# Kernel optimization log

Measured on AMD Instinct MI355X. Metric: run time of the kernel, lower is better.

## Reference

```python
import jax, jax.numpy as jnp
import numpy as np

B, S, D, H = 2, 2048, 1024, 16
DK = D // H
NEG = -1.0e9

def setup_inputs() -> dict:
    key = jax.random.key(0)
    ks = jax.random.split(key, 12)
    sc = 1.0 / np.sqrt(D)
    q = jax.random.normal(ks[0], (B, S, D), jnp.float32)
    k = jax.random.normal(ks[1], (B, S, D), jnp.float32)
    v = jax.random.normal(ks[2], (B, S, D), jnp.float32)
    # causal mask: True = masked (matches masked_fill(mask == True, -1e9))
    mask = jnp.broadcast_to(jnp.triu(jnp.ones((S, S), bool), k=1)[None, None], (B, 1, S, S))
    Wq = jax.random.normal(ks[3], (D, D), jnp.float32) * sc
    bq = jnp.zeros((D,), jnp.float32)
    Wk = jax.random.normal(ks[4], (D, D), jnp.float32) * sc
    bk = jnp.zeros((D,), jnp.float32)
    Wv = jax.random.normal(ks[5], (D, D), jnp.float32) * sc
    bv = jnp.zeros((D,), jnp.float32)
    Wo = jax.random.normal(ks[6], (D, D), jnp.float32) * sc
    bo = jnp.zeros((D,), jnp.float32)
    return {"q": q, "k": k, "v": v, "mask": mask,
            "Wq": Wq, "bq": bq, "Wk": Wk, "bk": bk,
            "Wv": Wv, "bv": bv, "Wo": Wo, "bo": bo}

def reference(q, k, v, mask, Wq, bq, Wk, bk, Wv, bv, Wo, bo):
    def split_heads(x):  # [B,S,D] -> [B,H,S,DK]
        return x.reshape(B, S, H, DK).transpose(0, 2, 1, 3)
    qh = split_heads(q @ Wq + bq)
    kh = split_heads(k @ Wk + bk)
    vh = split_heads(v @ Wv + bv)
    scores = jnp.einsum('bhqd,bhkd->bhqk', qh, kh) / np.sqrt(DK)
    scores = jnp.where(mask, NEG, scores)
    p = jax.nn.softmax(scores, axis=-1)
    out = jnp.einsum('bhqk,bhkd->bhqd', p, vh)  # [B,H,S,DK]
    out = out.transpose(0, 2, 1, 3).reshape(B, S, D)
    return out @ Wo + bo
```

## Files before the change

kernel.cpp:

```cpp
#include <hip/hip_runtime.h>

#define BB 2
#define SS 2048
#define DD 1024
#define HH 16
#define DKK 64

typedef __attribute__((ext_vector_type(8))) short short8;
typedef __attribute__((ext_vector_type(4))) float floatx4;

__device__ inline float bf2f(ushort u) {
    union { unsigned int i; float f; } x; x.i = ((unsigned int)u) << 16; return x.f;
}
__device__ inline ushort f2bf(float f) {
    union { float f; unsigned int i; } x; x.f = f;
    unsigned int r = x.i + 0x7fff + ((x.i >> 16) & 1);
    return (ushort)(r >> 16);
}
__device__ inline void async_cp16(const ushort* g, ushort* l) {
    __builtin_amdgcn_global_load_lds(
        (const __attribute__((address_space(1))) unsigned int*)g,
        (__attribute__((address_space(3))) unsigned int*)l, 16, 0, 0);
}
__device__ inline unsigned int cvt_pk_bf16(float lo, float hi) {
    unsigned int r;
    asm("v_cvt_pk_bf16_f32 %0, %1, %2" : "=v"(r) : "v"(lo), "v"(hi));
    return r;
}
__device__ inline void swap32(unsigned int& a, unsigned int& b) {
    asm("v_permlane32_swap_b32 %0, %1" : "+v"(a), "+v"(b));
}
__device__ inline void swap16(unsigned int& a, unsigned int& b) {
    asm("v_permlane16_swap_b32 %0, %1" : "+v"(a), "+v"(b));
}

__global__ __launch_bounds__(256) void cvt_w4(const float* __restrict__ w0,
                                              const float* __restrict__ w1,
                                              const float* __restrict__ w2,
                                              const float* __restrict__ w3,
                                              ushort* __restrict__ o0,
                                              ushort* __restrict__ o1,
                                              ushort* __restrict__ o2,
                                              ushort* __restrict__ o3) {
    __shared__ ushort t[32][33];
    int z = blockIdx.z;
    const float* in = (z == 0) ? w0 : (z == 1) ? w1 : (z == 2) ? w2 : w3;
    ushort* out = (z == 0) ? o0 : (z == 1) ? o1 : (z == 2) ? o2 : o3;
    int bx = blockIdx.x, by = blockIdx.y, tx = threadIdx.x;
    for (int i = threadIdx.y; i < 32; i += 8)
        t[i][tx] = f2bf(in[(size_t)(by * 32 + i) * DD + bx * 32 + tx]);
    __syncthreads();
    for (int i = threadIdx.y; i < 32; i += 8)
        out[(size_t)(bx * 32 + i) * DD + by * 32 + tx] = t[tx][i];
}

__global__ __launch_bounds__(256) void cvt_qkv(const float* __restrict__ q,
                                               const float* __restrict__ k,
                                               const float* __restrict__ v,
                                               ushort* __restrict__ oq,
                                               ushort* __restrict__ ok,
                                               ushort* __restrict__ ov) {
    int z = blockIdx.z;
    const float* in = (z == 0) ? q : (z == 1) ? k : v;
    ushort* out = (z == 0) ? oq : (z == 1) ? ok : ov;
    int i = blockIdx.x * 256 + threadIdx.x;
    float4 f0 = ((const float4*)in)[i * 2];
    float4 f1 = ((const float4*)in)[i * 2 + 1];
    short8 p;
    p[0] = (short)f2bf(f0.x); p[1] = (short)f2bf(f0.y);
    p[2] = (short)f2bf(f0.z); p[3] = (short)f2bf(f0.w);
    p[4] = (short)f2bf(f1.x); p[5] = (short)f2bf(f1.y);
    p[6] = (short)f2bf(f1.z); p[7] = (short)f2bf(f1.w);
    ((short8*)out)[i] = p;
}

__global__ __launch_bounds__(256) void gemm_qkv(const ushort* __restrict__ Xq,
                                                const ushort* __restrict__ Xk,
                                                const ushort* __restrict__ Xv,
                                                const ushort* __restrict__ WtQ,
                                                const ushort* __restrict__ WtK,
                                                const ushort* __restrict__ WtV,
                                                const float* __restrict__ bq,
                                                const float* __restrict__ bk,
                                                const float* __restrict__ bv,
                                                ushort* __restrict__ qh,
                                                ushort* __restrict__ kh,
                                                ushort* __restrict__ vt) {
    constexpr int K = 1024;
    constexpr int LDT = 136;
    __shared__ ushort smem[128 * LDT];
    ushort* Asm = smem;
    ushort* Bsm = smem + 4096;

    int lin = blockIdx.x + ((blockIdx.y + (blockIdx.z << 5)) << 3);
    int wid = (lin & 7) * 96 + (lin >> 3);
    int z = wid >> 8;
    int rem = wid & 255;
    int by = rem >> 3, bx = rem & 7;

    const ushort* A  = (z == 0) ? Xq : (z == 1) ? Xk : Xv;
    const ushort* Bt = (z == 0) ? WtQ : (z == 1) ? WtK : WtV;
    const float* bias = (z == 0) ? bq : (z == 1) ? bk : bv;
    ushort* outp = (z == 0) ? qh : (z == 1) ? kh : vt;

    int tid = threadIdx.x;
    int wave = tid >> 6, lane = tid & 63, quad = lane >> 4, l15 = lane & 15;
    int wm = wave >> 1, wn = wave & 1;
    int rowBase = by * 128, colBase = bx * 128;

    floatx4 acc[4][4] = {};
    for (int k0 = 0; k0 < K; k0 += 32) {
#pragma unroll
        for (int j = 0; j < 2; ++j) {
            int cbase = (j * 4 + wave) * 64;
            int c = cbase + lane;
            int row = c >> 2, sub = (c & 3) * 8;
            async_cp16(&A[(size_t)(rowBase + row) * K + k0 + sub], &Asm[cbase * 8]);
            async_cp16(&Bt[(size_t)(colBase + row) * K + k0 + sub], &Bsm[cbase * 8]);
        }
        __syncthreads();
        short8 af[4], bf[4];
#pragma unroll
        for (int mi = 0; mi < 4; ++mi)
            af[mi] = *(const short8*)&Asm[(wm * 64 + mi * 16 + l15) * 32 + quad * 8];
#pragma unroll
        for (int ni = 0; ni < 4; ++ni)
            bf[ni] = *(const short8*)&Bsm[(wn * 64 + ni * 16 + l15) * 32 + quad * 8];
#pragma unroll
        for (int mi = 0; mi < 4; ++mi)
#pragma unroll
            for (int ni = 0; ni < 4; ++ni)
                acc[mi][ni] = __builtin_amdgcn_mfma_f32_16x16x32_bf16(
                    af[mi], bf[ni], acc[mi][ni], 0, 0, 0);
        __syncthreads();
    }
    if (z == 2) {
        for (int mi = 0; mi < 4; ++mi)
            for (int ni = 0; ni < 4; ++ni) {
                int c = wn * 64 + ni * 16 + l15;
                float bv = bias[colBase + c];
                for (int i = 0; i < 4; ++i) {
                    int r = wm * 64 + mi * 16 + quad * 4 + i;
                    smem[c * LDT + r] = f2bf(acc[mi][ni][i] + bv);
                }
            }
        __syncthreads();
        int b = rowBase >> 11;
        int sBase = rowBase & 2047;
#pragma unroll
        for (int u = 0; u < 8; ++u) {
            int chunk = u * 256 + tid;
            int c = chunk >> 4;
            int r = (chunk & 15) * 8;
            int col = colBase + c, h = col >> 6, dk = col & 63;
            int4 val = *(const int4*)&smem[c * LDT + r];
            *(int4*)&outp[((size_t)((b * HH + h) * DKK + dk)) * SS + sBase + r] = val;
        }
    } else {
        for (int mi = 0; mi < 4; ++mi)
            for (int ni = 0; ni < 4; ++ni) {
                int c = wn * 64 + ni * 16 + l15;
                float bv = bias[colBase + c];
                for (int i = 0; i < 4; ++i) {
                    int r = wm * 64 + mi * 16 + quad * 4 + i;
                    smem[r * LDT + c] = f2bf(acc[mi][ni][i] + bv);
                }
            }
        __syncthreads();
        int bb = rowBase >> 11;
        int sBase = rowBase & 2047;
#pragma unroll
        for (int u = 0; u < 8; ++u) {
            int chunk = u * 256 + tid;
            int r = chunk >> 4;
            int cc = (chunk & 15) * 8;
            int col = colBase + cc, hh = col >> 6, dk = col & 63;
            int4 val = *(const int4*)&smem[r * LDT + cc];
            *(int4*)&outp[((size_t)((bb * HH + hh) * SS + sBase + r)) * DKK + dk] = val;
        }
    }
}

__global__ __launch_bounds__(256) void gemm_fin(const ushort* __restrict__ A,
                                                const ushort* __restrict__ Bt,
                                                const float* __restrict__ bias,
                                                float* __restrict__ outp) {
    constexpr int K = 1024, N = 1024;
    __shared__ ushort Asm[64 * 32];
    __shared__ ushort Bsm[128 * 32];
    int tid = threadIdx.x;
    int wave = tid >> 6, lane = tid & 63, quad = lane >> 4, l15 = lane & 15;
    int wm = wave >> 1, wn = wave & 1;

    int lin = blockIdx.x + (blockIdx.y << 3);
    int wid = (lin & 7) * 64 + (lin >> 3);
    int bx = wid & 7, by = wid >> 3;
    int rowBase = by * 64, colBase = bx * 128;

    floatx4 acc[2][4] = {};
    for (int k0 = 0; k0 < K; k0 += 32) {
#pragma unroll
        for (int j = 0; j < 3; ++j) {
            int c = j * 4 + wave;
            int cbase = (c < 4) ? c * 64 : (c - 4) * 64;
            int cc = cbase + lane;
            int row = cc >> 2, sub = (cc & 3) * 8;
            if (c < 4)
                async_cp16(&A[(size_t)(rowBase + row) * K + k0 + sub], &Asm[cbase * 8]);
            else
                async_cp16(&Bt[(size_t)(colBase + row) * K + k0 + sub], &Bsm[cbase * 8]);
        }
        __syncthreads();
        short8 af[2], bf[4];
#pragma unroll
        for (int mi = 0; mi < 2; ++mi)
            af[mi] = *(const short8*)&Asm[(wm * 32 + mi * 16 + l15) * 32 + quad * 8];
#pragma unroll
        for (int ni = 0; ni < 4; ++ni)
            bf[ni] = *(const short8*)&Bsm[(wn * 64 + ni * 16 + l15) * 32 + quad * 8];
#pragma unroll
        for (int mi = 0; mi < 2; ++mi)
#pragma unroll
            for (int ni = 0; ni < 4; ++ni)
                acc[mi][ni] = __builtin_amdgcn_mfma_f32_16x16x32_bf16(
                    af[mi], bf[ni], acc[mi][ni], 0, 0, 0);
        __syncthreads();
    }
    for (int mi = 0; mi < 2; ++mi)
        for (int ni = 0; ni < 4; ++ni) {
            int col = colBase + wn * 64 + ni * 16 + l15;
            float bv = bias[col];
            for (int i = 0; i < 4; ++i) {
                int row = rowBase + wm * 32 + mi * 16 + quad * 4 + i;
                outp[(size_t)row * N + col] = acc[mi][ni][i] + bv;
            }
        }
}

__global__ __launch_bounds__(256, 2) void flash_attn5(const ushort* __restrict__ qh,
                                                      const ushort* __restrict__ kh,
                                                      const ushort* __restrict__ vt,
                                                      ushort* __restrict__ attn) {
    constexpr int LD = 72;
    __shared__ ushort Ksm[2][64 * LD];
    __shared__ ushort Vsm[2][64 * LD];
    int tid = threadIdx.x;
    int h = blockIdx.y, b = blockIdx.z;
    int wave = tid >> 6, lane = tid & 63, quad = lane >> 4, l15 = lane & 15;
    const size_t headQK = ((size_t)(b * HH + h)) * SS * DKK;
    const size_t headV  = ((size_t)(b * HH + h)) * DKK * SS;
    int c0 = tid, r0 = c0 >> 3, s0 = (c0 & 7) * 8;
    int c1 = tid + 256, r1 = c1 >> 3, s1 = (c1 & 7) * 8;
    const int qt0 = blockIdx.x;
    const int qt1 = 31 - qt0;

    int qrow0 = qt0 * 64 + wave * 16 + l15;
    int qrow1 = qt1 * 64 + wave * 16 + l15;
    short8 q0a = *(const short8*)&qh[headQK + (size_t)qrow0 * DKK + quad * 8];
    short8 q0b = *(const short8*)&qh[headQK + (size_t)qrow0 * DKK + 32 + quad * 8];
    short8 q1a = *(const short8*)&qh[headQK + (size_t)qrow1 * DKK + quad * 8];
    short8 q1b = *(const short8*)&qh[headQK + (size_t)qrow1 * DKK + 32 + quad * 8];

    floatx4 o0[4] = {}, o1[4] = {};
    float l0 = 0.f, l1 = 0.f;
    int qsel = wave * 16 + l15;

    *(int4*)&Ksm[0][r0 * LD + s0] = *(const int4*)&kh[headQK + (size_t)r0 * DKK + s0];
    *(int4*)&Ksm[0][r1 * LD + s1] = *(const int4*)&kh[headQK + (size_t)r1 * DKK + s1];
    *(int4*)&Vsm[0][r0 * LD + s0] = *(const int4*)&vt[headV + (size_t)r0 * SS + s0];
    *(int4*)&Vsm[0][r1 * LD + s1] = *(const int4*)&vt[headV + (size_t)r1 * SS + s1];
    __syncthreads();

    for (int kt = 0; kt <= qt1; ++kt) {
        int cur = kt & 1;
        bool pre = (kt < qt1);
        bool act0 = (kt <= qt0);
        int4 kA, kB, vA, vB;
        if (pre) {
            const ushort* kp = &kh[headQK + (size_t)((kt + 1) * 64) * DKK];
            const ushort* vp = &vt[headV + (kt + 1) * 64];
            kA = *(const int4*)&kp[(size_t)r0 * DKK + s0];
            kB = *(const int4*)&kp[(size_t)r1 * DKK + s1];
            vA = *(const int4*)&vp[(size_t)r0 * SS + s0];
            vB = *(const int4*)&vp[(size_t)r1 * SS + s1];
        }
        floatx4 sv1[4], sv0[4];
#pragma unroll
        for (int cn = 0; cn < 4; ++cn) {
            short8 kf0 = *(const short8*)&Ksm[cur][(cn * 16 + l15) * LD + quad * 8];
            short8 kf1 = *(const short8*)&Ksm[cur][(cn * 16 + l15) * LD + 32 + quad * 8];
            floatx4 z = {};
            z = __builtin_amdgcn_mfma_f32_16x16x32_bf16(kf0, q1a, z, 0, 0, 0);
            z = __builtin_amdgcn_mfma_f32_16x16x32_bf16(kf1, q1b, z, 0, 0, 0);
            sv1[cn] = z;
            if (act0) {
                floatx4 y = {};
                y = __builtin_amdgcn_mfma_f32_16x16x32_bf16(kf0, q0a, y, 0, 0, 0);
                y = __builtin_amdgcn_mfma_f32_16x16x32_bf16(kf1, q0b, y, 0, 0, 0);
                sv0[cn] = y;
            }
        }
        short8 vf[2][4];
#pragma unroll
        for (int ks = 0; ks < 2; ++ks)
#pragma unroll
            for (int n = 0; n < 4; ++n)
                vf[ks][n] = *(const short8*)&Vsm[cur][(n * 16 + l15) * LD + ks * 32 + quad * 8];

        {
            bool diag = (kt == qt1);
            unsigned int pkd[4][2];
#pragma unroll
            for (int cn = 0; cn < 4; ++cn) {
#pragma unroll
                for (int i = 0; i < 4; ++i) {
                    float p = __expf(sv1[cn][i] * 0.125f);
                    if (diag && (cn * 16 + quad * 4 + i) > qsel) p = 0.f;
                    sv1[cn][i] = p;
                    l1 += p;
                }
                pkd[cn][0] = cvt_pk_bf16(sv1[cn][0], sv1[cn][1]);
                pkd[cn][1] = cvt_pk_bf16(sv1[cn][2], sv1[cn][3]);
            }
#pragma unroll
            for (int ks = 0; ks < 2; ++ks) {
                unsigned int a0 = pkd[ks * 2][0], b0 = pkd[ks * 2 + 1][0];
                swap32(a0, b0); swap16(a0, b0);
                unsigned int a1 = pkd[ks * 2][1], b1 = pkd[ks * 2 + 1][1];
                swap32(a1, b1); swap16(a1, b1);
                union { int4 i4; short8 s8; } u;
                u.i4 = make_int4((int)a0, (int)a1, (int)b0, (int)b1);
#pragma unroll
                for (int n = 0; n < 4; ++n)
                    o1[n] = __builtin_amdgcn_mfma_f32_16x16x32_bf16(
                        vf[ks][n], u.s8, o1[n], 0, 0, 0);
            }
        }
        if (act0) {
            bool diag = (kt == qt0);
            unsigned int pkd[4][2];
#pragma unroll
            for (int cn = 0; cn < 4; ++cn) {
#pragma unroll
                for (int i = 0; i < 4; ++i) {
                    float p = __expf(sv0[cn][i] * 0.125f);
                    if (diag && (cn * 16 + quad * 4 + i) > qsel) p = 0.f;
                    sv0[cn][i] = p;
                    l0 += p;
                }
                pkd[cn][0] = cvt_pk_bf16(sv0[cn][0], sv0[cn][1]);
                pkd[cn][1] = cvt_pk_bf16(sv0[cn][2], sv0[cn][3]);
            }
#pragma unroll
            for (int ks = 0; ks < 2; ++ks) {
                unsigned int a0 = pkd[ks * 2][0], b0 = pkd[ks * 2 + 1][0];
                swap32(a0, b0); swap16(a0, b0);
                unsigned int a1 = pkd[ks * 2][1], b1 = pkd[ks * 2 + 1][1];
                swap32(a1, b1); swap16(a1, b1);
                union { int4 i4; short8 s8; } u;
                u.i4 = make_int4((int)a0, (int)a1, (int)b0, (int)b1);
#pragma unroll
                for (int n = 0; n < 4; ++n)
                    o0[n] = __builtin_amdgcn_mfma_f32_16x16x32_bf16(
                        vf[ks][n], u.s8, o0[n], 0, 0, 0);
            }
        }
        if (pre) {
            int nb = cur ^ 1;
            *(int4*)&Ksm[nb][r0 * LD + s0] = kA;
            *(int4*)&Ksm[nb][r1 * LD + s1] = kB;
            *(int4*)&Vsm[nb][r0 * LD + s0] = vA;
            *(int4*)&Vsm[nb][r1 * LD + s1] = vB;
        }
        __syncthreads();
    }
    l0 += __shfl_xor(l0, 16, 64); l0 += __shfl_xor(l0, 32, 64);
    l1 += __shfl_xor(l1, 16, 64); l1 += __shfl_xor(l1, 32, 64);
    float inv0 = 1.0f / l0, inv1 = 1.0f / l1;
    size_t rowOff0 = ((size_t)(b * SS + qt0 * 64 + wave * 16 + l15)) * DD + h * 64;
    size_t rowOff1 = ((size_t)(b * SS + qt1 * 64 + wave * 16 + l15)) * DD + h * 64;
#pragma unroll
    for (int n = 0; n < 4; ++n) {
        int dof = n * 16 + quad * 4;
        int2 v0, v1;
        v0.x = (int)cvt_pk_bf16(o0[n][0] * inv0, o0[n][1] * inv0);
        v0.y = (int)cvt_pk_bf16(o0[n][2] * inv0, o0[n][3] * inv0);
        v1.x = (int)cvt_pk_bf16(o1[n][0] * inv1, o1[n][1] * inv1);
        v1.y = (int)cvt_pk_bf16(o1[n][2] * inv1, o1[n][3] * inv1);
        *(int2*)&attn[rowOff0 + dof] = v0;
        *(int2*)&attn[rowOff1 + dof] = v1;
    }
}

extern "C" void kernel_launch(void* const* d_in, const int* in_sizes, int n_in,
                              void* d_out, int out_size, void* d_ws, size_t ws_size,
                              hipStream_t stream) {
    const float* q  = (const float*)d_in[0];
    const float* k  = (const float*)d_in[1];
    const float* v  = (const float*)d_in[2];
    const float* Wq = (const float*)d_in[4];
    const float* bq = (const float*)d_in[5];
    const float* Wk = (const float*)d_in[6];
    const float* bk = (const float*)d_in[7];
    const float* Wv = (const float*)d_in[8];
    const float* bv = (const float*)d_in[9];
    const float* Wo = (const float*)d_in[10];
    const float* bo = (const float*)d_in[11];

    ushort* ws   = (ushort*)d_ws;
    ushort* WtQ  = ws;
    ushort* WtK  = WtQ + (1u << 20);
    ushort* WtV  = WtK + (1u << 20);
    ushort* WtO  = WtV + (1u << 20);
    ushort* Xv   = WtO + (1u << 20);
    ushort* qh   = Xv + (4u << 20);
    ushort* kh   = qh + (4u << 20);
    ushort* vt   = kh + (4u << 20);
    ushort* Xq   = (ushort*)d_out;
    ushort* Xk   = Xq + (4u << 20);
    ushort* attn = Xv;

    cvt_w4<<<dim3(32, 32, 4), dim3(32, 8), 0, stream>>>(Wq, Wk, Wv, Wo,
                                                        WtQ, WtK, WtV, WtO);
    cvt_qkv<<<dim3(2048, 1, 3), 256, 0, stream>>>(q, k, v, Xq, Xk, Xv);

    gemm_qkv<<<dim3(8, 32, 3), 256, 0, stream>>>(Xq, Xk, Xv, WtQ, WtK, WtV,
                                                 bq, bk, bv, qh, kh, vt);

    flash_attn5<<<dim3(16, 16, 2), 256, 0, stream>>>(qh, kh, vt, attn);

    gemm_fin<<<dim3(8, 64), 256, 0, stream>>>(attn, WtO, bo, (float*)d_out);
}
```

Before: 251.0 us.

## Double-buffer LDS tiles in QKV and output projection GEMMs

Both projection GEMMs now stage K-tiles into two alternating shared-memory buffers, issuing the async global-to-LDS copy for the next tile before computing on the current one. The aim is to overlap global load latency with MFMA work instead of stalling on a barrier after every load. One barrier per iteration remains, and LDS use per block grows, which may lower occupancy for the output GEMM. Correctness depends on the remaining end-of-loop barrier and on the async copies being complete before the next tile is read.

```diff
diff --git a/kernel.cpp b/kernel.cpp
--- a/kernel.cpp
+++ b/kernel.cpp
@@ -87,10 +87,9 @@
                                                 ushort* __restrict__ kh,
                                                 ushort* __restrict__ vt) {
     constexpr int K = 1024;
+    constexpr int NT = 32;
     constexpr int LDT = 136;
     __shared__ ushort smem[128 * LDT];
-    ushort* Asm = smem;
-    ushort* Bsm = smem + 4096;
 
     int lin = blockIdx.x + ((blockIdx.y + (blockIdx.z << 5)) << 3);
     int wid = (lin & 7) * 96 + (lin >> 3);
@@ -108,24 +107,31 @@
     int wm = wave >> 1, wn = wave & 1;
     int rowBase = by * 128, colBase = bx * 128;
 
-    floatx4 acc[4][4] = {};
-    for (int k0 = 0; k0 < K; k0 += 32) {
+    auto stage = [&](int k0, int d) {
+        int ab = d * 8192, bb2 = 4096 + d * 8192;
 #pragma unroll
         for (int j = 0; j < 2; ++j) {
             int cbase = (j * 4 + wave) * 64;
             int c = cbase + lane;
             int row = c >> 2, sub = (c & 3) * 8;
-            async_cp16(&A[(size_t)(rowBase + row) * K + k0 + sub], &Asm[cbase * 8]);
-            async_cp16(&Bt[(size_t)(colBase + row) * K + k0 + sub], &Bsm[cbase * 8]);
-        }
-        __syncthreads();
+            async_cp16(&A[(size_t)(rowBase + row) * K + k0 + sub], &smem[ab + cbase * 8]);
+            async_cp16(&Bt[(size_t)(colBase + row) * K + k0 + sub], &smem[bb2 + cbase * 8]);
+        }
+    };
+
+    floatx4 acc[4][4] = {};
+    stage(0, 0);
+    __syncthreads();
+    for (int t = 0; t < NT; ++t) {
+        if (t + 1 < NT) stage((t + 1) * 32, (t + 1) & 1);
+        int ab = (t & 1) * 8192, bb2 = 4096 + (t & 1) * 8192;
         short8 af[4], bf[4];
 #pragma unroll
         for (int mi = 0; mi < 4; ++mi)
-            af[mi] = *(const short8*)&Asm[(wm * 64 + mi * 16 + l15) * 32 + quad * 8];
+            af[mi] = *(const short8*)&smem[ab + (wm * 64 + mi * 16 + l15) * 32 + quad * 8];
 #pragma unroll
         for (int ni = 0; ni < 4; ++ni)
-            bf[ni] = *(const short8*)&Bsm[(wn * 64 + ni * 16 + l15) * 32 + quad * 8];
+            bf[ni] = *(const short8*)&smem[bb2 + (wn * 64 + ni * 16 + l15) * 32 + quad * 8];
 #pragma unroll
         for (int mi = 0; mi < 4; ++mi)
 #pragma unroll
@@ -185,9 +191,8 @@
                                                 const ushort* __restrict__ Bt,
                                                 const float* __restrict__ bias,
                                                 float* __restrict__ outp) {
-    constexpr int K = 1024, N = 1024;
-    __shared__ ushort Asm[64 * 32];
-    __shared__ ushort Bsm[128 * 32];
+    constexpr int K = 1024, N = 1024, NT = 32;
+    __shared__ ushort smem[12288];
     int tid = threadIdx.x;
     int wave = tid >> 6, lane = tid & 63, quad = lane >> 4, l15 = lane & 15;
     int wm = wave >> 1, wn = wave & 1;
@@ -197,8 +202,8 @@
     int bx = wid & 7, by = wid >> 3;
     int rowBase = by * 64, colBase = bx * 128;
 
-    floatx4 acc[2][4] = {};
-    for (int k0 = 0; k0 < K; k0 += 32) {
+    auto stage = [&](int k0, int d) {
+        int ab = d * 6144, bb2 = 2048 + d * 6144;
 #pragma unroll
         for (int j = 0; j < 3; ++j) {
             int c = j * 4 + wave;
@@ -206,18 +211,25 @@
             int cc = cbase + lane;
             int row = cc >> 2, sub = (cc & 3) * 8;
             if (c < 4)
-                async_cp16(&A[(size_t)(rowBase + row) * K + k0 + sub], &Asm[cbase * 8]);
+                async_cp16(&A[(size_t)(rowBase + row) * K + k0 + sub], &smem[ab + cbase * 8]);
             else
-                async_cp16(&Bt[(size_t)(colBase + row) * K + k0 + sub], &Bsm[cbase * 8]);
-        }
-        __syncthreads();
+                async_cp16(&Bt[(size_t)(colBase + row) * K + k0 + sub], &smem[bb2 + cbase * 8]);
+        }
+    };
+
+    floatx4 acc[2][4] = {};
+    stage(0, 0);
+    __syncthreads();
+    for (int t = 0; t < NT; ++t) {
+        if (t + 1 < NT) stage((t + 1) * 32, (t + 1) & 1);
+        int ab = (t & 1) * 6144, bb2 = 2048 + (t & 1) * 6144;
         short8 af[2], bf[4];
 #pragma unroll
         for (int mi = 0; mi < 2; ++mi)
-            af[mi] = *(const short8*)&Asm[(wm * 32 + mi * 16 + l15) * 32 + quad * 8];
+            af[mi] = *(const short8*)&smem[ab + (wm * 32 + mi * 16 + l15) * 32 + quad * 8];
 #pragma unroll
         for (int ni = 0; ni < 4; ++ni)
-            bf[ni] = *(const short8*)&Bsm[(wn * 64 + ni * 16 + l15) * 32 + quad * 8];
+            bf[ni] = *(const short8*)&smem[bb2 + (wn * 64 + ni * 16 + l15) * 32 + quad * 8];
 #pragma unroll
         for (int mi = 0; mi < 2; ++mi)
 #pragma unroll
```

Result: faster. 246.0 us (-2.0%).
